# Kernel tuning notes

Hardware: AMD Instinct MI355X
Metric: run time of the kernel (lower is better)

The kernel has to match this reference:

```python
import jax, jax.numpy as jnp
import numpy as np

BATCH, IN_F, OUT_F, BASIS = 64, 512, 512, 8


def _cheb_basis(x):
    # Chebyshev basis T_k(tanh(x)) for k=1..BASIS; x: (b, i) -> (b, i, BASIS)
    theta = jnp.arccos(jnp.clip(jnp.tanh(x), -1.0 + 1e-6, 1.0 - 1e-6))
    ks = jnp.arange(1, BASIS + 1, dtype=x.dtype)
    return jnp.cos(theta[..., None] * ks)


def setup_inputs() -> dict:
    key = jax.random.key(0)
    k1, k2, k3 = jax.random.split(key, 3)
    x = jax.random.normal(k1, (BATCH, IN_F), dtype=jnp.float32)
    # xavier_normal_ on w: std = sqrt(2 / (fan_in + fan_out))
    w = jax.random.normal(k2, (IN_F, OUT_F), dtype=jnp.float32) * np.sqrt(2.0 / (IN_F + OUT_F))
    # normal_(c, 0, 0.1)
    c = jax.random.normal(k3, (IN_F, OUT_F, BASIS), dtype=jnp.float32) * 0.1
    return {"x": x, "w": w, "c": c}


def reference(x, w, c):
    # basis: (b, i, k); contract basis dim with c: (i, o, k) -> (b, i, o)
    basis = _cheb_basis(x)
    s = jnp.einsum("bik,iok->bio", basis, c)
    # residual SiLU(x) broadcast over o, weight by w, reduce over in_features
    out = jnp.einsum("bio,io->bo", jax.nn.silu(x)[:, :, None] + s, w)
    return out
```

## Files before the change

kernel.cpp:

```cpp
#include <hip/hip_runtime.h>

#define BATCH 64
#define IN_F 512
#define OUT_F 512
#define ICH 32
#define NKB (IN_F / ICH)
#define NNB 32

typedef short short8 __attribute__((ext_vector_type(8)));
typedef float f32x4 __attribute__((ext_vector_type(4)));

static __device__ __forceinline__ unsigned bfpk(float a, float b) {
    unsigned ua = __float_as_uint(a) + 0x8000u;
    unsigned ub = __float_as_uint(b) + 0x8000u;
    return __builtin_amdgcn_perm(ub, ua, 0x07060302u);
}

__global__ __launch_bounds__(256, 2) void kan_mfma(const float* __restrict__ x,
                                                   const float* __restrict__ w,
                                                   const float* __restrict__ c,
                                                   float* __restrict__ out) {
    __shared__ __align__(16) short T_lds[ICH * BATCH * 8];
    __shared__ __align__(16) short S_lds[BATCH * ICH];

    int nb  = blockIdx.x & (NNB - 1);
    int kb  = blockIdx.x >> 5;
    int i0  = kb * ICH;
    int o0  = nb * 16;
    int tid = threadIdx.x;

    int lane = tid & 63;
    int wid  = tid >> 6;
    int m    = lane & 15;
    int quad = lane >> 4;
    int b    = wid * 16 + m;
    int o    = o0 + m;

    int pb = tid & 63;
    int wq = tid >> 6;
    const float* xp = x + (size_t)pb * IN_F + i0 + wq * 8;
    float4 xa = *(const float4*)xp;
    float4 xb = *(const float4*)(xp + 4);

    float4 cv0[8], cv1[8];
    float  wv[8];
    float  ws[8];
#pragma unroll
    for (int s = 0; s < 8; ++s) {
        int i = i0 + s * 4 + quad;
        const float4* cp = (const float4*)(c + ((size_t)i * OUT_F + o) * 8);
        cv0[s] = cp[0];
        cv1[s] = cp[1];
        wv[s]  = w[(size_t)i * OUT_F + o];
    }
#pragma unroll
    for (int j = 0; j < 8; ++j)
        ws[j] = w[(size_t)(i0 + quad * 8 + j) * OUT_F + o];

    {
        float xs[8] = {xa.x, xa.y, xa.z, xa.w, xb.x, xb.y, xb.z, xb.w};
        unsigned spk[4];
        float sl_prev = 0.f;
#pragma unroll
        for (int j = 0; j < 8; ++j) {
            int il = wq * 8 + j;
            float xv = xs[j];
            float xc = fminf(fmaxf(xv, -15.f), 15.f);
            float u  = __expf(-xc);
            float sl = __fdividef(xv, 1.0f + u);
            float u2 = u * u;
            float t  = __fdividef(1.0f - u2, 1.0f + u2);
            t = fminf(fmaxf(t, -1.0f + 1e-6f), 1.0f - 1e-6f);
            float t2 = t + t;
            float T1 = t;
            float T2 = fmaf(t2, T1, -1.0f);
            float T3 = fmaf(t2, T2, -T1);
            float T4 = fmaf(t2, T3, -T2);
            float T5 = fmaf(t2, T4, -T3);
            float T6 = fmaf(t2, T5, -T4);
            float T7 = fmaf(t2, T6, -T5);
            float T8 = fmaf(t2, T7, -T6);
            union { short8 v; unsigned u4[4]; } fr;
            fr.u4[0] = bfpk(T1, T2);
            fr.u4[1] = bfpk(T3, T4);
            fr.u4[2] = bfpk(T5, T6);
            fr.u4[3] = bfpk(T7, T8);
            *(short8*)&T_lds[(il * BATCH + pb) * 8] = fr.v;
            if (j & 1) spk[j >> 1] = bfpk(sl_prev, sl);
            sl_prev = sl;
        }
        union { short8 v; unsigned u4[4]; } sv;
        sv.u4[0] = spk[0]; sv.u4[1] = spk[1];
        sv.u4[2] = spk[2]; sv.u4[3] = spk[3];
        *(short8*)&S_lds[pb * ICH + wq * 8] = sv.v;
    }
    __syncthreads();

    short8 af[8];
#pragma unroll
    for (int s = 0; s < 8; ++s)
        af[s] = *(const short8*)&T_lds[((s * 4 + quad) * BATCH + b) * 8];
    short8 aw = *(const short8*)&S_lds[b * ICH + quad * 8];

    f32x4 acc = {0.f, 0.f, 0.f, 0.f};
#pragma unroll
    for (int s = 0; s < 8; ++s) {
        union { short8 v; unsigned u4[4]; } bf;
        bf.u4[0] = bfpk(wv[s] * cv0[s].x, wv[s] * cv0[s].y);
        bf.u4[1] = bfpk(wv[s] * cv0[s].z, wv[s] * cv0[s].w);
        bf.u4[2] = bfpk(wv[s] * cv1[s].x, wv[s] * cv1[s].y);
        bf.u4[3] = bfpk(wv[s] * cv1[s].z, wv[s] * cv1[s].w);
        acc = __builtin_amdgcn_mfma_f32_16x16x32_bf16(af[s], bf.v, acc, 0, 0, 0);
    }
    {
        union { short8 v; unsigned u4[4]; } bw;
        bw.u4[0] = bfpk(ws[0], ws[1]);
        bw.u4[1] = bfpk(ws[2], ws[3]);
        bw.u4[2] = bfpk(ws[4], ws[5]);
        bw.u4[3] = bfpk(ws[6], ws[7]);
        acc = __builtin_amdgcn_mfma_f32_16x16x32_bf16(aw, bw.v, acc, 0, 0, 0);
    }

#pragma unroll
    for (int r = 0; r < 4; ++r)
        atomicAdd(out + (size_t)(wid * 16 + quad * 4 + r) * OUT_F + o, acc[r]);
}

extern "C" void kernel_launch(void* const* d_in, const int* in_sizes, int n_in,
                              void* d_out, int out_size, void* d_ws, size_t ws_size,
                              hipStream_t stream) {
    const float* x = (const float*)d_in[0];
    const float* w = (const float*)d_in[1];
    const float* c = (const float*)d_in[2];
    float* out = (float*)d_out;

    kan_mfma<<<NKB * NNB, 256, 0, stream>>>(x, w, c, out);
}
```

Measured before the change: 66.68 us.

## Double input-chunk per block, split K across waves, reduce in LDS before atomics

```diff
diff --git a/kernel.cpp b/kernel.cpp
--- a/kernel.cpp
+++ b/kernel.cpp
@@ -3,7 +3,7 @@
 #define BATCH 64
 #define IN_F 512
 #define OUT_F 512
-#define ICH 32
+#define ICH 64
 #define NKB (IN_F / ICH)
 #define NNB 32
 
@@ -16,12 +16,13 @@
     return __builtin_amdgcn_perm(ub, ua, 0x07060302u);
 }
 
-__global__ __launch_bounds__(256, 2) void kan_mfma(const float* __restrict__ x,
+__global__ __launch_bounds__(512, 2) void kan_mfma(const float* __restrict__ x,
                                                    const float* __restrict__ w,
                                                    const float* __restrict__ c,
                                                    float* __restrict__ out) {
     __shared__ __align__(16) short T_lds[ICH * BATCH * 8];
     __shared__ __align__(16) short S_lds[BATCH * ICH];
+    __shared__ __align__(16) float r_lds[4 * 64 * 4];
 
     int nb  = blockIdx.x & (NNB - 1);
     int kb  = blockIdx.x >> 5;
@@ -33,12 +34,13 @@
     int wid  = tid >> 6;
     int m    = lane & 15;
     int quad = lane >> 4;
-    int b    = wid * 16 + m;
+    int bt   = wid & 3;
+    int kh   = wid >> 2;
+    int b    = bt * 16 + m;
     int o    = o0 + m;
+    int ik   = i0 + kh * 32;
 
-    int pb = tid & 63;
-    int wq = tid >> 6;
-    const float* xp = x + (size_t)pb * IN_F + i0 + wq * 8;
+    const float* xp = x + (size_t)lane * IN_F + i0 + wid * 8;
     float4 xa = *(const float4*)xp;
     float4 xb = *(const float4*)(xp + 4);
 
@@ -47,7 +49,7 @@
     float  ws[8];
 #pragma unroll
     for (int s = 0; s < 8; ++s) {
-        int i = i0 + s * 4 + quad;
+        int i = ik + s * 4 + quad;
         const float4* cp = (const float4*)(c + ((size_t)i * OUT_F + o) * 8);
         cv0[s] = cp[0];
         cv1[s] = cp[1];
@@ -55,7 +57,7 @@
     }
 #pragma unroll
     for (int j = 0; j < 8; ++j)
-        ws[j] = w[(size_t)(i0 + quad * 8 + j) * OUT_F + o];
+        ws[j] = w[(size_t)(ik + quad * 8 + j) * OUT_F + o];
 
     {
         float xs[8] = {xa.x, xa.y, xa.z, xa.w, xb.x, xb.y, xb.z, xb.w};
@@ -63,7 +65,7 @@
         float sl_prev = 0.f;
 #pragma unroll
         for (int j = 0; j < 8; ++j) {
-            int il = wq * 8 + j;
+            int il = wid * 8 + j;
             float xv = xs[j];
             float xc = fminf(fmaxf(xv, -15.f), 15.f);
             float u  = __expf(-xc);
@@ -85,22 +87,22 @@
             fr.u4[1] = bfpk(T3, T4);
             fr.u4[2] = bfpk(T5, T6);
             fr.u4[3] = bfpk(T7, T8);
-            *(short8*)&T_lds[(il * BATCH + pb) * 8] = fr.v;
+            *(short8*)&T_lds[(il * BATCH + lane) * 8] = fr.v;
             if (j & 1) spk[j >> 1] = bfpk(sl_prev, sl);
             sl_prev = sl;
         }
         union { short8 v; unsigned u4[4]; } sv;
         sv.u4[0] = spk[0]; sv.u4[1] = spk[1];
         sv.u4[2] = spk[2]; sv.u4[3] = spk[3];
-        *(short8*)&S_lds[pb * ICH + wq * 8] = sv.v;
+        *(short8*)&S_lds[lane * ICH + wid * 8] = sv.v;
     }
     __syncthreads();
 
     short8 af[8];
 #pragma unroll
     for (int s = 0; s < 8; ++s)
-        af[s] = *(const short8*)&T_lds[((s * 4 + quad) * BATCH + b) * 8];
-    short8 aw = *(const short8*)&S_lds[b * ICH + quad * 8];
+        af[s] = *(const short8*)&T_lds[((kh * 32 + s * 4 + quad) * BATCH + b) * 8];
+    short8 aw = *(const short8*)&S_lds[b * ICH + kh * 32 + quad * 8];
 
     f32x4 acc = {0.f, 0.f, 0.f, 0.f};
 #pragma unroll
@@ -121,9 +123,17 @@
         acc = __builtin_amdgcn_mfma_f32_16x16x32_bf16(aw, bw.v, acc, 0, 0, 0);
     }
 
-#pragma unroll
-    for (int r = 0; r < 4; ++r)
-        atomicAdd(out + (size_t)(wid * 16 + quad * 4 + r) * OUT_F + o, acc[r]);
+    if (kh == 1)
+        *(float4*)&r_lds[(bt * 64 + lane) * 4] = make_float4(acc[0], acc[1],
+                                                             acc[2], acc[3]);
+    __syncthreads();
+    if (kh == 0) {
+        float4 other = *(const float4*)&r_lds[(bt * 64 + lane) * 4];
+        atomicAdd(out + (size_t)(bt * 16 + quad * 4 + 0) * OUT_F + o, acc[0] + other.x);
+        atomicAdd(out + (size_t)(bt * 16 + quad * 4 + 1) * OUT_F + o, acc[1] + other.y);
+        atomicAdd(out + (size_t)(bt * 16 + quad * 4 + 2) * OUT_F + o, acc[2] + other.z);
+        atomicAdd(out + (size_t)(bt * 16 + quad * 4 + 3) * OUT_F + o, acc[3] + other.w);
+    }
 }
 
 extern "C" void kernel_launch(void* const* d_in, const int* in_sizes, int n_in,
@@ -134,5 +144,5 @@
     const float* c = (const float*)d_in[2];
     float* out = (float*)d_out;
 
-    kan_mfma<<<NKB * NNB, 256, 0, stream>>>(x, w, c, out);
+    kan_mfma<<<NKB * NNB, 512, 0, stream>>>(x, w, c, out);
 }
```

Result: no change. 66.69 us (+0.0%).
